# Kernel tuning notes

Hardware: AMD Instinct MI355X
Metric: run time of the kernel (lower is better)

Reference implementation:

```python
import jax, jax.numpy as jnp
import numpy as np

HEADS = 16
DIM = 1024
HEAD_DIM = DIM // HEADS


def setup_inputs() -> dict:
    key = jax.random.key(0)
    k1, k2 = jax.random.split(key)
    images = jax.random.normal(k1, (2, 2048, DIM), dtype=jnp.float32)
    # torch nn.Linear(dim, 3*dim, bias=False): y = x @ W.T, W: [3*dim, dim].
    # Store as [dim, 3*dim] for direct x @ W_qkv.
    W_qkv = jax.random.normal(k2, (DIM, 3 * DIM), dtype=jnp.float32) / np.sqrt(DIM)
    return {"images": images, "W_qkv": W_qkv}


def reference(images, W_qkv):
    B, S, D = images.shape
    qkv = images @ W_qkv  # [B, S, 3D]
    q, k, v = jnp.split(qkv, 3, axis=-1)
    # [B, S, H, Dh] -> [B, H, S, Dh]
    def to_heads(t):
        return t.reshape(B, S, HEADS, HEAD_DIM).transpose(0, 2, 1, 3)
    q, k, v = to_heads(q), to_heads(k), to_heads(v)
    scale = 1.0 / jnp.sqrt(jnp.asarray(HEAD_DIM, dtype=q.dtype))
    scores = jnp.einsum('bhqd,bhkd->bhqk', q, k) * scale  # [B, H, S, S]
    probs = jax.nn.softmax(scores, axis=-1)
    out = jnp.einsum('bhqk,bhkd->bhqd', probs, v)  # [B, H, S, Dh]
    return out.transpose(0, 2, 1, 3).reshape(B, S, D)
```

## Files before the change

### kernel.cpp

```cpp
#include <hip/hip_runtime.h>
#include <hip/hip_bf16.h>
#include <math.h>

typedef __bf16 bf16x8 __attribute__((ext_vector_type(8)));
typedef float f32x4 __attribute__((ext_vector_type(4)));
typedef unsigned short u16x8 __attribute__((ext_vector_type(8)));
typedef unsigned short u16;

#define S_LEN 2048
#define DMODEL 1024
#define NH 16

__device__ __forceinline__ u16 f2bf(float f) {
    __bf16 b = (__bf16)f;
    return __builtin_bit_cast(u16, b);
}
__device__ __forceinline__ float bf2f(u16 u) {
    union { unsigned int i; float f; } v; v.i = ((unsigned int)u) << 16; return v.f;
}

__device__ __forceinline__ void gload16(const u16* g, u16* lds_base) {
    __builtin_amdgcn_global_load_lds(
        (const __attribute__((address_space(1))) unsigned int*)g,
        (__attribute__((address_space(3))) unsigned int*)lds_base,
        16, 0, 0);
}

__global__ __launch_bounds__(256) void cvt_x(const float* __restrict__ in, u16* __restrict__ outp) {
    int i = (blockIdx.x * 256 + threadIdx.x) * 4;
    float4 v = *(const float4*)(in + i);
    outp[i + 0] = f2bf(v.x); outp[i + 1] = f2bf(v.y);
    outp[i + 2] = f2bf(v.z); outp[i + 3] = f2bf(v.w);
}

__global__ __launch_bounds__(256) void transpose_w(const float* __restrict__ W, u16* __restrict__ Wt) {
    __shared__ u16 tile[32][33];
    int n0 = blockIdx.x * 32, k0 = blockIdx.y * 32;
    int tx = threadIdx.x & 31, ty = threadIdx.x >> 5;
#pragma unroll
    for (int i = 0; i < 4; i++) {
        int k = ty + i * 8;
        tile[k][tx] = f2bf(W[(size_t)(k0 + k) * 3072 + n0 + tx]);
    }
    __syncthreads();
#pragma unroll
    for (int i = 0; i < 4; i++) {
        int n = ty + i * 8;
        Wt[(size_t)(n0 + n) * 1024 + k0 + tx] = tile[tx][n];
    }
}

__global__ __launch_bounds__(256) void qkv_gemm(const u16* __restrict__ A, const u16* __restrict__ Bt,
                                                u16* __restrict__ C) {
    __shared__ alignas(16) u16 As[128 * 64];
    __shared__ alignas(16) u16 Bs[128 * 64];
    const int tid = threadIdx.x, l = tid & 63, w = tid >> 6;
    const int bm = blockIdx.y, bn = blockIdx.x;
    const int wm = w >> 1, wn = w & 1;
    const int c0 = l & 15, g = l >> 4;
    f32x4 acc[4][4] = {};
    for (int kt = 0; kt < 1024; kt += 64) {
        __syncthreads();
#pragma unroll
        for (int n = 0; n < 4; n++) {
            int i = tid + n * 256;
            int r = i >> 3, c = i & 7;
            int cs = c ^ (r & 7);
            u16* dstA = As + (size_t)(w * 64 + n * 256) * 8;
            u16* dstB = Bs + (size_t)(w * 64 + n * 256) * 8;
            gload16(A + (size_t)(bm * 128 + r) * 1024 + kt + cs * 8, dstA);
            gload16(Bt + (size_t)(bn * 128 + r) * 1024 + kt + cs * 8, dstB);
        }
        __syncthreads();
#pragma unroll
        for (int kk = 0; kk < 2; kk++) {
            bf16x8 af[4], bfr[4];
#pragma unroll
            for (int m = 0; m < 4; m++) {
                int row = wm * 64 + m * 16 + c0;
                af[m] = *(const bf16x8*)((const char*)As + row * 128 + (((g + kk * 4) ^ (row & 7)) << 4));
            }
#pragma unroll
            for (int n = 0; n < 4; n++) {
                int row = wn * 64 + n * 16 + c0;
                bfr[n] = *(const bf16x8*)((const char*)Bs + row * 128 + (((g + kk * 4) ^ (row & 7)) << 4));
            }
#pragma unroll
            for (int m = 0; m < 4; m++)
#pragma unroll
                for (int n = 0; n < 4; n++)
                    acc[m][n] = __builtin_amdgcn_mfma_f32_16x16x32_bf16(af[m], bfr[n], acc[m][n], 0, 0, 0);
        }
    }
#pragma unroll
    for (int m = 0; m < 4; m++)
#pragma unroll
        for (int n = 0; n < 4; n++)
#pragma unroll
            for (int j = 0; j < 4; j++) {
                int row = bm * 128 + wm * 64 + m * 16 + 4 * g + j;
                int col = bn * 128 + wn * 64 + n * 16 + c0;
                C[(size_t)row * 3072 + col] = f2bf(acc[m][n][j]);
            }
}

__global__ __launch_bounds__(256) void transpose_v(const u16* __restrict__ QKV, u16* __restrict__ Vtp) {
    __shared__ u16 tile[64][72];
    const int bh = blockIdx.x >> 5, st = blockIdx.x & 31;
    const int b = bh >> 4, h = bh & 15;
    const u16* src = QKV + (size_t)b * S_LEN * 3072 + 2048 + h * 64;
    const int sl = threadIdx.x >> 2;
    const int cg = (threadIdx.x & 3) * 16;
#pragma unroll
    for (int ii = 0; ii < 2; ii++) {
        u16x8 v = *(const u16x8*)(src + (size_t)(st * 64 + sl) * 3072 + cg + ii * 8);
        *(u16x8*)&tile[sl][cg + ii * 8] = v;
    }
    __syncthreads();
    const int dl = threadIdx.x >> 2;
#pragma unroll
    for (int ii = 0; ii < 2; ii++) {
        u16x8 o;
#pragma unroll
        for (int q = 0; q < 8; q++) {
            int p = cg + ii * 8 + q;
            int kb = 2 * (p >> 5) + ((p >> 2) & 1);
            int t = kb * 16 + ((p >> 3) & 3) * 4 + (p & 3);
            o[q] = tile[t][dl];
        }
        *(u16x8*)(Vtp + ((size_t)bh * 64 + dl) * S_LEN + st * 64 + cg + ii * 8) = o;
    }
}

__global__ __launch_bounds__(256, 4) void attn4(const u16* __restrict__ QKV, const u16* __restrict__ Vtp,
                                                float* __restrict__ out) {
    __shared__ alignas(16) u16 Ks[2][64 * 64];
    __shared__ alignas(16) u16 Vs[2][64 * 64];
    const int bid = blockIdx.x;
    const int wg = ((bid & 7) << 7) | (bid >> 3);
    const int tid = threadIdx.x, l = tid & 63, w = tid >> 6;
    const int qt = wg & 31, bh = wg >> 5;
    const int b = bh >> 4, h = bh & 15;
    const int c0 = l & 15, g = l >> 4;
    const u16* Qb = QKV + (size_t)b * S_LEN * 3072 + h * 64;
    const u16* Kb = Qb + 1024;
    const u16* Vb = Vtp + (size_t)bh * 64 * S_LEN;
    const int qrow = qt * 64 + w * 16 + c0;

    const int i0 = tid, i1 = tid + 256;
    const int r0 = i0 >> 3, cs0 = (i0 & 7) ^ (r0 & 7);
    const int r1 = i1 >> 3, cs1 = (i1 & 7) ^ (r1 & 7);

    bf16x8 qf[2];
    {
        const float qs = 0.125f * 1.44269504f;
#pragma unroll
        for (int kk = 0; kk < 2; kk++) {
            u16x8 v = *(const u16x8*)(Qb + (size_t)qrow * 3072 + kk * 32 + g * 8);
            bf16x8 q;
#pragma unroll
            for (int j = 0; j < 8; j++) q[j] = (__bf16)(bf2f(v[j]) * qs);
            qf[kk] = q;
        }
    }
    float m_r = -INFINITY, l_r = 0.f;
    f32x4 accO[4] = {};

    gload16(Kb + (size_t)r0 * 3072 + cs0 * 8, Ks[0] + (size_t)(w * 64) * 8);
    gload16(Kb + (size_t)r1 * 3072 + cs1 * 8, Ks[0] + (size_t)(w * 64 + 256) * 8);
    gload16(Vb + (size_t)r0 * S_LEN + cs0 * 8, Vs[0] + (size_t)(w * 64) * 8);
    gload16(Vb + (size_t)r1 * S_LEN + cs1 * 8, Vs[0] + (size_t)(w * 64 + 256) * 8);

    for (int t = 0; t < 32; t++) {
        const int cur = t & 1;
        __syncthreads();
        if (t + 1 < 32) {
            const int kvn = (t + 1) * 64;
            gload16(Kb + (size_t)(kvn + r0) * 3072 + cs0 * 8, Ks[cur ^ 1] + (size_t)(w * 64) * 8);
            gload16(Kb + (size_t)(kvn + r1) * 3072 + cs1 * 8, Ks[cur ^ 1] + (size_t)(w * 64 + 256) * 8);
            gload16(Vb + (size_t)r0 * S_LEN + kvn + cs0 * 8, Vs[cur ^ 1] + (size_t)(w * 64) * 8);
            gload16(Vb + (size_t)r1 * S_LEN + kvn + cs1 * 8, Vs[cur ^ 1] + (size_t)(w * 64 + 256) * 8);
        }
        bf16x8 vf[2][4];
#pragma unroll
        for (int kk = 0; kk < 2; kk++)
#pragma unroll
            for (int n = 0; n < 4; n++) {
                int d = n * 16 + c0;
                vf[kk][n] = *(const bf16x8*)((const char*)Vs[cur] + d * 128 + (((g + 4 * kk) ^ (d & 7)) << 4));
            }
        f32x4 sc[4] = {};
        __builtin_amdgcn_s_setprio(1);
#pragma unroll
        for (int kb = 0; kb < 4; kb++) {
            int key = kb * 16 + c0;
#pragma unroll
            for (int kk = 0; kk < 2; kk++) {
                bf16x8 kf = *(const bf16x8*)((const char*)Ks[cur] + key * 128 + (((g + kk * 4) ^ (key & 7)) << 4));
                sc[kb] = __builtin_amdgcn_mfma_f32_16x16x32_bf16(kf, qf[kk], sc[kb], 0, 0, 0);
            }
        }
        __builtin_amdgcn_s_setprio(0);
        float m0 = fmaxf(fmaxf(sc[0][0], sc[0][1]), sc[0][2]);
        float m1 = fmaxf(fmaxf(sc[0][3], sc[1][0]), sc[1][1]);
        float m2 = fmaxf(fmaxf(sc[1][2], sc[1][3]), sc[2][0]);
        float m3 = fmaxf(fmaxf(sc[2][1], sc[2][2]), sc[2][3]);
        float m4 = fmaxf(fmaxf(sc[3][0], sc[3][1]), sc[3][2]);
        float mx = fmaxf(fmaxf(fmaxf(m0, m1), m2), fmaxf(fmaxf(m3, m4), sc[3][3]));
        mx = fmaxf(mx, __shfl_xor(mx, 16));
        mx = fmaxf(mx, __shfl_xor(mx, 32));
        if (!__all(mx <= m_r + 8.f)) {
            float mnew = fmaxf(m_r, mx);
            float alpha = __builtin_amdgcn_exp2f(m_r - mnew);
            l_r *= alpha;
            m_r = mnew;
#pragma unroll
            for (int j = 0; j < 4; j++) {
                float aj = __shfl(alpha, 20 * g + j);
#pragma unroll
                for (int n = 0; n < 4; n++) accO[n][j] *= aj;
            }
        }
        float ps = 0.f;
#pragma unroll
        for (int kb = 0; kb < 4; kb++)
#pragma unroll
            for (int j = 0; j < 4; j++) {
                float p = __builtin_amdgcn_exp2f(sc[kb][j] - m_r);
                sc[kb][j] = p;
                ps += p;
            }
        ps += __shfl_xor(ps, 16);
        ps += __shfl_xor(ps, 32);
        l_r += ps;
        __builtin_amdgcn_s_setprio(1);
#pragma unroll
        for (int kk = 0; kk < 2; kk++) {
            bf16x8 pf;
#pragma unroll
            for (int j = 0; j < 4; j++) {
                pf[j]     = (__bf16)sc[2 * kk][j];
                pf[j + 4] = (__bf16)sc[2 * kk + 1][j];
            }
#pragma unroll
            for (int n = 0; n < 4; n++)
                accO[n] = __builtin_amdgcn_mfma_f32_16x16x32_bf16(pf, vf[kk][n], accO[n], 0, 0, 0);
        }
        __builtin_amdgcn_s_setprio(0);
    }
#pragma unroll
    for (int j = 0; j < 4; j++) {
        float inv = 1.0f / __shfl(l_r, 20 * g + j);
        int row = qt * 64 + w * 16 + 4 * g + j;
#pragma unroll
        for (int n = 0; n < 4; n++)
            out[((size_t)b * S_LEN + row) * DMODEL + h * 64 + n * 16 + c0] = accO[n][j] * inv;
    }
}

extern "C" void kernel_launch(void* const* d_in, const int* in_sizes, int n_in,
                              void* d_out, int out_size, void* d_ws, size_t ws_size,
                              hipStream_t stream) {
    const float* X = (const float*)d_in[0];
    const float* W = (const float*)d_in[1];
    float* out = (float*)d_out;

    u16* Xb  = (u16*)d_ws;
    u16* Wt  = Xb + (size_t)4096 * 1024;
    u16* QKV = Wt + (size_t)3072 * 1024;
    u16* Vtp = QKV + (size_t)4096 * 3072;

    cvt_x<<<4096, 256, 0, stream>>>(X, Xb);
    transpose_w<<<dim3(96, 32), 256, 0, stream>>>(W, Wt);
    qkv_gemm<<<dim3(24, 32), 256, 0, stream>>>(Xb, Wt, QKV);
    transpose_v<<<1024, 256, 0, stream>>>(QKV, Vtp);
    attn4<<<1024, 256, 0, stream>>>(QKV, Vtp, out);
}
```

Measured before the change: 113.7 us.

## Process two query sub-tiles per wave and compute row sums via MFMA

The attention kernel drops from 4 waves to 2 waves per block, and each wave now handles 32 query rows as two 16-row sub-tiles. Each K fragment read from LDS is reused for two MFMAs, which halves LDS traffic per FLOP. The softmax row sum is now accumulated by an extra MFMA against a ones vector instead of shuffle reductions, and the LDS offsets are precomputed. The cost is more registers per wave and fewer waves per block to hide latency.

```diff
diff --git a/kernel.cpp b/kernel.cpp
--- a/kernel.cpp
+++ b/kernel.cpp
@@ -132,7 +132,7 @@
     }
 }
 
-__global__ __launch_bounds__(256, 4) void attn4(const u16* __restrict__ QKV, const u16* __restrict__ Vtp,
+__global__ __launch_bounds__(128, 2) void attn5(const u16* __restrict__ QKV, const u16* __restrict__ Vtp,
                                                 float* __restrict__ out) {
     __shared__ alignas(16) u16 Ks[2][64 * 64];
     __shared__ alignas(16) u16 Vs[2][64 * 64];
@@ -145,117 +145,145 @@
     const u16* Qb = QKV + (size_t)b * S_LEN * 3072 + h * 64;
     const u16* Kb = Qb + 1024;
     const u16* Vb = Vtp + (size_t)bh * 64 * S_LEN;
-    const int qrow = qt * 64 + w * 16 + c0;
-
-    const int i0 = tid, i1 = tid + 256;
-    const int r0 = i0 >> 3, cs0 = (i0 & 7) ^ (r0 & 7);
-    const int r1 = i1 >> 3, cs1 = (i1 & 7) ^ (r1 & 7);
-
-    bf16x8 qf[2];
+
+    int rr[4], cc[4];
+#pragma unroll
+    for (int n = 0; n < 4; n++) {
+        int i = tid + n * 128;
+        rr[n] = i >> 3;
+        cc[n] = ((i & 7) ^ (rr[n] & 7)) * 8;
+    }
+
+    int koff[8], voff[8];
+#pragma unroll
+    for (int kb = 0; kb < 4; kb++)
+#pragma unroll
+        for (int kk = 0; kk < 2; kk++) {
+            int key = kb * 16 + c0;
+            koff[kb * 2 + kk] = key * 128 + (((g + kk * 4) ^ (key & 7)) << 4);
+        }
+#pragma unroll
+    for (int kk = 0; kk < 2; kk++)
+#pragma unroll
+        for (int n = 0; n < 4; n++) {
+            int d = n * 16 + c0;
+            voff[kk * 4 + n] = d * 128 + (((g + 4 * kk) ^ (d & 7)) << 4);
+        }
+
+    bf16x8 qf[2][2];
     {
         const float qs = 0.125f * 1.44269504f;
 #pragma unroll
-        for (int kk = 0; kk < 2; kk++) {
-            u16x8 v = *(const u16x8*)(Qb + (size_t)qrow * 3072 + kk * 32 + g * 8);
-            bf16x8 q;
-#pragma unroll
-            for (int j = 0; j < 8; j++) q[j] = (__bf16)(bf2f(v[j]) * qs);
-            qf[kk] = q;
-        }
-    }
-    float m_r = -INFINITY, l_r = 0.f;
-    f32x4 accO[4] = {};
-
-    gload16(Kb + (size_t)r0 * 3072 + cs0 * 8, Ks[0] + (size_t)(w * 64) * 8);
-    gload16(Kb + (size_t)r1 * 3072 + cs1 * 8, Ks[0] + (size_t)(w * 64 + 256) * 8);
-    gload16(Vb + (size_t)r0 * S_LEN + cs0 * 8, Vs[0] + (size_t)(w * 64) * 8);
-    gload16(Vb + (size_t)r1 * S_LEN + cs1 * 8, Vs[0] + (size_t)(w * 64 + 256) * 8);
+        for (int s = 0; s < 2; s++) {
+            int qrow = qt * 64 + w * 32 + s * 16 + c0;
+#pragma unroll
+            for (int kk = 0; kk < 2; kk++) {
+                u16x8 v = *(const u16x8*)(Qb + (size_t)qrow * 3072 + kk * 32 + g * 8);
+                bf16x8 q;
+#pragma unroll
+                for (int j = 0; j < 8; j++) q[j] = (__bf16)(bf2f(v[j]) * qs);
+                qf[s][kk] = q;
+            }
+        }
+    }
+    bf16x8 vone;
+#pragma unroll
+    for (int j = 0; j < 8; j++) vone[j] = (__bf16)1.0f;
+
+    float m_r[2] = {-INFINITY, -INFINITY};
+    f32x4 accO[2][4] = {};
+    f32x4 accL[2] = {};
+
+#pragma unroll
+    for (int n = 0; n < 4; n++) {
+        gload16(Kb + (size_t)rr[n] * 3072 + cc[n], Ks[0] + (size_t)(w * 64 + n * 128) * 8);
+        gload16(Vb + (size_t)rr[n] * S_LEN + cc[n], Vs[0] + (size_t)(w * 64 + n * 128) * 8);
+    }
 
     for (int t = 0; t < 32; t++) {
         const int cur = t & 1;
         __syncthreads();
         if (t + 1 < 32) {
             const int kvn = (t + 1) * 64;
-            gload16(Kb + (size_t)(kvn + r0) * 3072 + cs0 * 8, Ks[cur ^ 1] + (size_t)(w * 64) * 8);
-            gload16(Kb + (size_t)(kvn + r1) * 3072 + cs1 * 8, Ks[cur ^ 1] + (size_t)(w * 64 + 256) * 8);
-            gload16(Vb + (size_t)r0 * S_LEN + kvn + cs0 * 8, Vs[cur ^ 1] + (size_t)(w * 64) * 8);
-            gload16(Vb + (size_t)r1 * S_LEN + kvn + cs1 * 8, Vs[cur ^ 1] + (size_t)(w * 64 + 256) * 8);
-        }
+#pragma unroll
+            for (int n = 0; n < 4; n++) {
+                gload16(Kb + (size_t)(kvn + rr[n]) * 3072 + cc[n], Ks[cur ^ 1] + (size_t)(w * 64 + n * 128) * 8);
+                gload16(Vb + (size_t)rr[n] * S_LEN + kvn + cc[n], Vs[cur ^ 1] + (size_t)(w * 64 + n * 128) * 8);
+            }
+        }
+        const char* Kc = (const char*)Ks[cur];
+        const char* Vc = (const char*)Vs[cur];
+        f32x4 sc[2][4] = {};
+        __builtin_amdgcn_s_setprio(1);
+#pragma unroll
+        for (int kb = 0; kb < 4; kb++)
+#pragma unroll
+            for (int kk = 0; kk < 2; kk++) {
+                bf16x8 kf = *(const bf16x8*)(Kc + koff[kb * 2 + kk]);
+                sc[0][kb] = __builtin_amdgcn_mfma_f32_16x16x32_bf16(kf, qf[0][kk], sc[0][kb], 0, 0, 0);
+                sc[1][kb] = __builtin_amdgcn_mfma_f32_16x16x32_bf16(kf, qf[1][kk], sc[1][kb], 0, 0, 0);
+            }
+        __builtin_amdgcn_s_setprio(0);
         bf16x8 vf[2][4];
 #pragma unroll
         for (int kk = 0; kk < 2; kk++)
 #pragma unroll
-            for (int n = 0; n < 4; n++) {
-                int d = n * 16 + c0;
-                vf[kk][n] = *(const bf16x8*)((const char*)Vs[cur] + d * 128 + (((g + 4 * kk) ^ (d & 7)) << 4));
-            }
-        f32x4 sc[4] = {};
-        __builtin_amdgcn_s_setprio(1);
-#pragma unroll
-        for (int kb = 0; kb < 4; kb++) {
-            int key = kb * 16 + c0;
+            for (int n = 0; n < 4; n++)
+                vf[kk][n] = *(const bf16x8*)(Vc + voff[kk * 4 + n]);
+#pragma unroll
+        for (int s = 0; s < 2; s++) {
+            float m0 = fmaxf(fmaxf(sc[s][0][0], sc[s][0][1]), sc[s][0][2]);
+            float m1 = fmaxf(fmaxf(sc[s][0][3], sc[s][1][0]), sc[s][1][1]);
+            float m2 = fmaxf(fmaxf(sc[s][1][2], sc[s][1][3]), sc[s][2][0]);
+            float m3 = fmaxf(fmaxf(sc[s][2][1], sc[s][2][2]), sc[s][2][3]);
+            float m4 = fmaxf(fmaxf(sc[s][3][0], sc[s][3][1]), sc[s][3][2]);
+            float mx = fmaxf(fmaxf(fmaxf(m0, m1), m2), fmaxf(fmaxf(m3, m4), sc[s][3][3]));
+            mx = fmaxf(mx, __shfl_xor(mx, 16));
+            mx = fmaxf(mx, __shfl_xor(mx, 32));
+            if (!__all(mx <= m_r[s] + 8.f)) {
+                float mnew = fmaxf(m_r[s], mx);
+                float alpha = __builtin_amdgcn_exp2f(m_r[s] - mnew);
+                m_r[s] = mnew;
+#pragma unroll
+                for (int j = 0; j < 4; j++) {
+                    float aj = __shfl(alpha, 20 * g + j);
+                    accL[s][j] *= aj;
+#pragma unroll
+                    for (int n = 0; n < 4; n++) accO[s][n][j] *= aj;
+                }
+            }
+#pragma unroll
+            for (int kb = 0; kb < 4; kb++)
+#pragma unroll
+                for (int j = 0; j < 4; j++)
+                    sc[s][kb][j] = __builtin_amdgcn_exp2f(sc[s][kb][j] - m_r[s]);
+            __builtin_amdgcn_s_setprio(1);
 #pragma unroll
             for (int kk = 0; kk < 2; kk++) {
-                bf16x8 kf = *(const bf16x8*)((const char*)Ks[cur] + key * 128 + (((g + kk * 4) ^ (key & 7)) << 4));
-                sc[kb] = __builtin_amdgcn_mfma_f32_16x16x32_bf16(kf, qf[kk], sc[kb], 0, 0, 0);
-            }
-        }
-        __builtin_amdgcn_s_setprio(0);
-        float m0 = fmaxf(fmaxf(sc[0][0], sc[0][1]), sc[0][2]);
-        float m1 = fmaxf(fmaxf(sc[0][3], sc[1][0]), sc[1][1]);
-        float m2 = fmaxf(fmaxf(sc[1][2], sc[1][3]), sc[2][0]);
-        float m3 = fmaxf(fmaxf(sc[2][1], sc[2][2]), sc[2][3]);
-        float m4 = fmaxf(fmaxf(sc[3][0], sc[3][1]), sc[3][2]);
-        float mx = fmaxf(fmaxf(fmaxf(m0, m1), m2), fmaxf(fmaxf(m3, m4), sc[3][3]));
-        mx = fmaxf(mx, __shfl_xor(mx, 16));
-        mx = fmaxf(mx, __shfl_xor(mx, 32));
-        if (!__all(mx <= m_r + 8.f)) {
-            float mnew = fmaxf(m_r, mx);
-            float alpha = __builtin_amdgcn_exp2f(m_r - mnew);
-            l_r *= alpha;
-            m_r = mnew;
-#pragma unroll
-            for (int j = 0; j < 4; j++) {
-                float aj = __shfl(alpha, 20 * g + j);
-#pragma unroll
-                for (int n = 0; n < 4; n++) accO[n][j] *= aj;
-            }
-        }
-        float ps = 0.f;
-#pragma unroll
-        for (int kb = 0; kb < 4; kb++)
-#pragma unroll
-            for (int j = 0; j < 4; j++) {
-                float p = __builtin_amdgcn_exp2f(sc[kb][j] - m_r);
-                sc[kb][j] = p;
-                ps += p;
-            }
-        ps += __shfl_xor(ps, 16);
-        ps += __shfl_xor(ps, 32);
-        l_r += ps;
-        __builtin_amdgcn_s_setprio(1);
-#pragma unroll
-        for (int kk = 0; kk < 2; kk++) {
-            bf16x8 pf;
-#pragma unroll
-            for (int j = 0; j < 4; j++) {
-                pf[j]     = (__bf16)sc[2 * kk][j];
-                pf[j + 4] = (__bf16)sc[2 * kk + 1][j];
-            }
+                bf16x8 pf;
+#pragma unroll
+                for (int j = 0; j < 4; j++) {
+                    pf[j]     = (__bf16)sc[s][2 * kk][j];
+                    pf[j + 4] = (__bf16)sc[s][2 * kk + 1][j];
+                }
+                accL[s] = __builtin_amdgcn_mfma_f32_16x16x32_bf16(pf, vone, accL[s], 0, 0, 0);
+#pragma unroll
+                for (int n = 0; n < 4; n++)
+                    accO[s][n] = __builtin_amdgcn_mfma_f32_16x16x32_bf16(pf, vf[kk][n], accO[s][n], 0, 0, 0);
+            }
+            __builtin_amdgcn_s_setprio(0);
+        }
+    }
+#pragma unroll
+    for (int s = 0; s < 2; s++)
+#pragma unroll
+        for (int j = 0; j < 4; j++) {
+            float inv = 1.0f / accL[s][j];
+            int row = qt * 64 + w * 32 + s * 16 + 4 * g + j;
 #pragma unroll
             for (int n = 0; n < 4; n++)
-                accO[n] = __builtin_amdgcn_mfma_f32_16x16x32_bf16(pf, vf[kk][n], accO[n], 0, 0, 0);
-        }
-        __builtin_amdgcn_s_setprio(0);
-    }
-#pragma unroll
-    for (int j = 0; j < 4; j++) {
-        float inv = 1.0f / __shfl(l_r, 20 * g + j);
-        int row = qt * 64 + w * 16 + 4 * g + j;
-#pragma unroll
-        for (int n = 0; n < 4; n++)
-            out[((size_t)b * S_LEN + row) * DMODEL + h * 64 + n * 16 + c0] = accO[n][j] * inv;
-    }
+                out[((size_t)b * S_LEN + row) * DMODEL + h * 64 + n * 16 + c0] = accO[s][n][j] * inv;
+        }
 }
 
 extern "C" void kernel_launch(void* const* d_in, const int* in_sizes, int n_in,
@@ -274,5 +302,5 @@
     transpose_w<<<dim3(96, 32), 256, 0, stream>>>(W, Wt);
     qkv_gemm<<<dim3(24, 32), 256, 0, stream>>>(Xb, Wt, QKV);
     transpose_v<<<1024, 256, 0, stream>>>(QKV, Vtp);
-    attn4<<<1024, 256, 0, stream>>>(QKV, Vtp, out);
-}
+    attn5<<<1024, 128, 0, stream>>>(QKV, Vtp, out);
+}
```

Result: no change. 112.7 us (-0.9%).

## Split KV range into two online-softmax streams and compute row sums via MFMA

Applied to the files above, without the earlier changes.

The attention kernel now treats each 64-key tile as two 32-key halves taken from separate halves of the sequence. Each half keeps its own running max and accumulators, and the two are merged with exp2 weights at the end. The row sum of probabilities is computed by an MFMA against a ones vector instead of shuffle reductions. LDS offsets are precomputed, and the occupancy hint is dropped from launch_bounds. The intent is to shorten the softmax dependency chain and cut cross-lane shuffles, at the cost of doubling the accumulator registers and adding extra rescale branches.

```diff
diff --git a/kernel.cpp b/kernel.cpp
--- a/kernel.cpp
+++ b/kernel.cpp
@@ -132,8 +132,8 @@
     }
 }
 
-__global__ __launch_bounds__(256, 4) void attn4(const u16* __restrict__ QKV, const u16* __restrict__ Vtp,
-                                                float* __restrict__ out) {
+__global__ __launch_bounds__(256) void attn7(const u16* __restrict__ QKV, const u16* __restrict__ Vtp,
+                                             float* __restrict__ outp) {
     __shared__ alignas(16) u16 Ks[2][64 * 64];
     __shared__ alignas(16) u16 Vs[2][64 * 64];
     const int bid = blockIdx.x;
@@ -147,9 +147,21 @@
     const u16* Vb = Vtp + (size_t)bh * 64 * S_LEN;
     const int qrow = qt * 64 + w * 16 + c0;
 
-    const int i0 = tid, i1 = tid + 256;
-    const int r0 = i0 >> 3, cs0 = (i0 & 7) ^ (r0 & 7);
+    const int r0 = tid >> 3, cs0 = (tid & 7) ^ (r0 & 7);
+    const int i1 = tid + 256;
     const int r1 = i1 >> 3, cs1 = (i1 & 7) ^ (r1 & 7);
+    const int krow0 = r0;
+    const int krow1 = 1024 + (r1 - 32);
+    const int vcol0 = (cs0 & 3) * 8 + (cs0 >> 2) * 1024;
+    const int vcol1 = (cs1 & 3) * 8 + (cs1 >> 2) * 1024;
+    const int dbA = (w * 64) * 8, dbB = (256 + w * 64) * 8;
+
+    int koff[8];
+#pragma unroll
+    for (int x = 0; x < 4; x++)
+#pragma unroll
+        for (int kk = 0; kk < 2; kk++)
+            koff[x * 2 + kk] = (x * 16 + c0) * 128 + (((g + kk * 4) ^ (c0 & 7)) << 4);
 
     bf16x8 qf[2];
     {
@@ -163,98 +175,117 @@
             qf[kk] = q;
         }
     }
-    float m_r = -INFINITY, l_r = 0.f;
-    f32x4 accO[4] = {};
-
-    gload16(Kb + (size_t)r0 * 3072 + cs0 * 8, Ks[0] + (size_t)(w * 64) * 8);
-    gload16(Kb + (size_t)r1 * 3072 + cs1 * 8, Ks[0] + (size_t)(w * 64 + 256) * 8);
-    gload16(Vb + (size_t)r0 * S_LEN + cs0 * 8, Vs[0] + (size_t)(w * 64) * 8);
-    gload16(Vb + (size_t)r1 * S_LEN + cs1 * 8, Vs[0] + (size_t)(w * 64 + 256) * 8);
+    bf16x8 vone;
+#pragma unroll
+    for (int j = 0; j < 8; j++) vone[j] = (__bf16)1.0f;
+
+    float m_a = -INFINITY, m_b = -INFINITY;
+    f32x4 accOa[4] = {}, accOb[4] = {};
+    f32x4 accLa = {}, accLb = {};
+
+    gload16(Kb + (size_t)krow0 * 3072 + cs0 * 8, Ks[0] + dbA);
+    gload16(Kb + (size_t)krow1 * 3072 + cs1 * 8, Ks[0] + dbB);
+    gload16(Vb + (size_t)r0 * S_LEN + vcol0, Vs[0] + dbA);
+    gload16(Vb + (size_t)r1 * S_LEN + vcol1, Vs[0] + dbB);
 
     for (int t = 0; t < 32; t++) {
         const int cur = t & 1;
         __syncthreads();
         if (t + 1 < 32) {
-            const int kvn = (t + 1) * 64;
-            gload16(Kb + (size_t)(kvn + r0) * 3072 + cs0 * 8, Ks[cur ^ 1] + (size_t)(w * 64) * 8);
-            gload16(Kb + (size_t)(kvn + r1) * 3072 + cs1 * 8, Ks[cur ^ 1] + (size_t)(w * 64 + 256) * 8);
-            gload16(Vb + (size_t)r0 * S_LEN + kvn + cs0 * 8, Vs[cur ^ 1] + (size_t)(w * 64) * 8);
-            gload16(Vb + (size_t)r1 * S_LEN + kvn + cs1 * 8, Vs[cur ^ 1] + (size_t)(w * 64 + 256) * 8);
-        }
-        bf16x8 vf[2][4];
-#pragma unroll
-        for (int kk = 0; kk < 2; kk++)
-#pragma unroll
-            for (int n = 0; n < 4; n++) {
-                int d = n * 16 + c0;
-                vf[kk][n] = *(const bf16x8*)((const char*)Vs[cur] + d * 128 + (((g + 4 * kk) ^ (d & 7)) << 4));
-            }
+            const int s0 = (t + 1) * 32;
+            gload16(Kb + (size_t)(s0 + krow0) * 3072 + cs0 * 8, Ks[cur ^ 1] + dbA);
+            gload16(Kb + (size_t)(s0 + krow1) * 3072 + cs1 * 8, Ks[cur ^ 1] + dbB);
+            gload16(Vb + (size_t)r0 * S_LEN + s0 + vcol0, Vs[cur ^ 1] + dbA);
+            gload16(Vb + (size_t)r1 * S_LEN + s0 + vcol1, Vs[cur ^ 1] + dbB);
+        }
+        const char* Kc = (const char*)Ks[cur];
+        const char* Vc = (const char*)Vs[cur];
         f32x4 sc[4] = {};
         __builtin_amdgcn_s_setprio(1);
 #pragma unroll
-        for (int kb = 0; kb < 4; kb++) {
-            int key = kb * 16 + c0;
+        for (int kb = 0; kb < 4; kb++)
 #pragma unroll
             for (int kk = 0; kk < 2; kk++) {
-                bf16x8 kf = *(const bf16x8*)((const char*)Ks[cur] + key * 128 + (((g + kk * 4) ^ (key & 7)) << 4));
+                bf16x8 kf = *(const bf16x8*)(Kc + koff[kb * 2 + kk]);
                 sc[kb] = __builtin_amdgcn_mfma_f32_16x16x32_bf16(kf, qf[kk], sc[kb], 0, 0, 0);
             }
-        }
         __builtin_amdgcn_s_setprio(0);
-        float m0 = fmaxf(fmaxf(sc[0][0], sc[0][1]), sc[0][2]);
-        float m1 = fmaxf(fmaxf(sc[0][3], sc[1][0]), sc[1][1]);
-        float m2 = fmaxf(fmaxf(sc[1][2], sc[1][3]), sc[2][0]);
-        float m3 = fmaxf(fmaxf(sc[2][1], sc[2][2]), sc[2][3]);
-        float m4 = fmaxf(fmaxf(sc[3][0], sc[3][1]), sc[3][2]);
-        float mx = fmaxf(fmaxf(fmaxf(m0, m1), m2), fmaxf(fmaxf(m3, m4), sc[3][3]));
-        mx = fmaxf(mx, __shfl_xor(mx, 16));
-        mx = fmaxf(mx, __shfl_xor(mx, 32));
-        if (!__all(mx <= m_r + 8.f)) {
-            float mnew = fmaxf(m_r, mx);
-            float alpha = __builtin_amdgcn_exp2f(m_r - mnew);
-            l_r *= alpha;
-            m_r = mnew;
+        bf16x8 vf[2][4];
+#pragma unroll
+        for (int kk = 0; kk < 2; kk++)
+#pragma unroll
+            for (int n = 0; n < 4; n++)
+                vf[kk][n] = *(const bf16x8*)(Vc + koff[n * 2 + kk]);
+        float mxA = fmaxf(fmaxf(fmaxf(sc[0][0], sc[0][1]), fmaxf(sc[0][2], sc[0][3])),
+                          fmaxf(fmaxf(sc[1][0], sc[1][1]), fmaxf(sc[1][2], sc[1][3])));
+        mxA = fmaxf(mxA, __shfl_xor(mxA, 16));
+        mxA = fmaxf(mxA, __shfl_xor(mxA, 32));
+        float mxB = fmaxf(fmaxf(fmaxf(sc[2][0], sc[2][1]), fmaxf(sc[2][2], sc[2][3])),
+                          fmaxf(fmaxf(sc[3][0], sc[3][1]), fmaxf(sc[3][2], sc[3][3])));
+        mxB = fmaxf(mxB, __shfl_xor(mxB, 16));
+        mxB = fmaxf(mxB, __shfl_xor(mxB, 32));
+        if (!__all(mxA <= m_a + 8.f)) {
+            float mnew = fmaxf(m_a, mxA);
+            float alpha = __builtin_amdgcn_exp2f(m_a - mnew);
+            m_a = mnew;
 #pragma unroll
             for (int j = 0; j < 4; j++) {
                 float aj = __shfl(alpha, 20 * g + j);
-#pragma unroll
-                for (int n = 0; n < 4; n++) accO[n][j] *= aj;
-            }
-        }
-        float ps = 0.f;
-#pragma unroll
-        for (int kb = 0; kb < 4; kb++)
-#pragma unroll
-            for (int j = 0; j < 4; j++) {
-                float p = __builtin_amdgcn_exp2f(sc[kb][j] - m_r);
-                sc[kb][j] = p;
-                ps += p;
-            }
-        ps += __shfl_xor(ps, 16);
-        ps += __shfl_xor(ps, 32);
-        l_r += ps;
+                accLa[j] *= aj;
+#pragma unroll
+                for (int n = 0; n < 4; n++) accOa[n][j] *= aj;
+            }
+        }
+        if (!__all(mxB <= m_b + 8.f)) {
+            float mnew = fmaxf(m_b, mxB);
+            float alpha = __builtin_amdgcn_exp2f(m_b - mnew);
+            m_b = mnew;
+#pragma unroll
+            for (int j = 0; j < 4; j++) {
+                float aj = __shfl(alpha, 20 * g + j);
+                accLb[j] *= aj;
+#pragma unroll
+                for (int n = 0; n < 4; n++) accOb[n][j] *= aj;
+            }
+        }
+#pragma unroll
+        for (int kb = 0; kb < 2; kb++)
+#pragma unroll
+            for (int j = 0; j < 4; j++) {
+                sc[kb][j]     = __builtin_amdgcn_exp2f(sc[kb][j] - m_a);
+                sc[kb + 2][j] = __builtin_amdgcn_exp2f(sc[kb + 2][j] - m_b);
+            }
         __builtin_amdgcn_s_setprio(1);
-#pragma unroll
-        for (int kk = 0; kk < 2; kk++) {
-            bf16x8 pf;
-#pragma unroll
-            for (int j = 0; j < 4; j++) {
-                pf[j]     = (__bf16)sc[2 * kk][j];
-                pf[j + 4] = (__bf16)sc[2 * kk + 1][j];
-            }
-#pragma unroll
-            for (int n = 0; n < 4; n++)
-                accO[n] = __builtin_amdgcn_mfma_f32_16x16x32_bf16(pf, vf[kk][n], accO[n], 0, 0, 0);
+        {
+            bf16x8 pfa, pfb;
+#pragma unroll
+            for (int j = 0; j < 4; j++) {
+                pfa[j] = (__bf16)sc[0][j]; pfa[j + 4] = (__bf16)sc[1][j];
+                pfb[j] = (__bf16)sc[2][j]; pfb[j + 4] = (__bf16)sc[3][j];
+            }
+            accLa = __builtin_amdgcn_mfma_f32_16x16x32_bf16(pfa, vone, accLa, 0, 0, 0);
+            accLb = __builtin_amdgcn_mfma_f32_16x16x32_bf16(pfb, vone, accLb, 0, 0, 0);
+#pragma unroll
+            for (int n = 0; n < 4; n++) {
+                accOa[n] = __builtin_amdgcn_mfma_f32_16x16x32_bf16(pfa, vf[0][n], accOa[n], 0, 0, 0);
+                accOb[n] = __builtin_amdgcn_mfma_f32_16x16x32_bf16(pfb, vf[1][n], accOb[n], 0, 0, 0);
+            }
         }
         __builtin_amdgcn_s_setprio(0);
     }
+    float mM = fmaxf(m_a, m_b);
+    float wA = __builtin_amdgcn_exp2f(m_a - mM);
+    float wB = __builtin_amdgcn_exp2f(m_b - mM);
 #pragma unroll
     for (int j = 0; j < 4; j++) {
-        float inv = 1.0f / __shfl(l_r, 20 * g + j);
+        float ajA = __shfl(wA, 20 * g + j);
+        float ajB = __shfl(wB, 20 * g + j);
+        float inv = 1.0f / (accLa[j] * ajA + accLb[j] * ajB);
         int row = qt * 64 + w * 16 + 4 * g + j;
+        float* op = outp + ((size_t)b * S_LEN + row) * DMODEL + h * 64;
 #pragma unroll
         for (int n = 0; n < 4; n++)
-            out[((size_t)b * S_LEN + row) * DMODEL + h * 64 + n * 16 + c0] = accO[n][j] * inv;
+            op[n * 16 + c0] = (accOa[n][j] * ajA + accOb[n][j] * ajB) * inv;
     }
 }
 
@@ -274,5 +305,5 @@
     transpose_w<<<dim3(96, 32), 256, 0, stream>>>(W, Wt);
     qkv_gemm<<<dim3(24, 32), 256, 0, stream>>>(Xb, Wt, QKV);
     transpose_v<<<1024, 256, 0, stream>>>(QKV, Vtp);
-    attn4<<<1024, 256, 0, stream>>>(QKV, Vtp, out);
-}
+    attn7<<<1024, 256, 0, stream>>>(QKV, Vtp, out);
+}
```

Result: slower. 139.6 us (+22.8%).
